# Optimization experiments

Hardware: AMD Instinct MI355X
Metric: run time of the kernel (lower is better)

The kernel has to match this reference:

```python
import jax, jax.numpy as jnp
import numpy as np
from jax import lax

DN = ('NCHW', 'OIHW', 'NCHW')

def _conv(x, w, b):
    y = lax.conv_general_dilated(x, w, (1, 1), 'SAME', dimension_numbers=DN)
    return y + b[None, :, None, None]

def setup_inputs() -> dict:
    key = jax.random.key(0)
    ks = jax.random.split(key, 12)
    B, C, H, W = 8, 32, 128, 128
    Cb, INT, K, FK = 64, 64, 3, 3
    inp = {
        'z': jax.random.normal(ks[0], (B, C, H, W), jnp.float32),
        'backbone': jax.random.normal(ks[1], (B, Cb, H, W), jnp.float32),
        'mem_stab': jax.random.normal(ks[2], (B, C, H, W), jnp.float32),
        'mem_unstab': jax.random.normal(ks[3], (B, C, H, W), jnp.float32),
        'w0': jax.random.normal(ks[4], (INT, Cb + 3 * C, K, K), jnp.float32) * 0.05,
        'b0': jnp.zeros((INT,), jnp.float32),
        'w1': jax.random.normal(ks[5], (INT, INT, K, K), jnp.float32) * 0.05,
        'b1': jnp.zeros((INT,), jnp.float32),
        'w2': jax.random.normal(ks[6], (INT, INT, K, K), jnp.float32) * 0.05,
        'b2': jnp.zeros((INT,), jnp.float32),
        'w_last': jax.random.normal(ks[7], (C * FK * FK, INT, K, K), jnp.float32) * 0.05,
        'b_last': jnp.full((C * FK * FK,), -4.0, jnp.float32),
        'fusion_kernel_size': FK,
    }
    return inp

def reference(z, backbone, mem_stab, mem_unstab, w0, b0, w1, b1, w2, b2, w_last, b_last, fusion_kernel_size):
    B, C, H, W = z.shape
    k = int(fusion_kernel_size)
    p = k * k
    # controller conv stack (LeakyReLU slope 0.01, matching nn.LeakyReLU default)
    q = jnp.concatenate([backbone, z, mem_stab, mem_unstab], axis=1)
    q = jax.nn.leaky_relu(_conv(q, w0, b0), 0.01)
    q = jax.nn.leaky_relu(_conv(q, w1, b1), 0.01)
    q = jax.nn.leaky_relu(_conv(q, w2, b2), 0.01)
    # fusion head -> [B, C, p, HW]
    head = _conv(q, w_last, b_last).reshape(B, C, p, H * W)
    # softmax over p kernel positions + one extra logit-0 slot for z itself
    eta = jax.nn.softmax(jnp.concatenate([head, jnp.zeros_like(head[:, :, :1])], axis=2), axis=2)
    # unfold(mem_stab, k, padding=k//2): patches ordered (c, kh, kw) like torch unfold
    pad = k // 2
    mpad = jnp.pad(mem_stab, ((0, 0), (0, 0), (pad, pad), (pad, pad)))
    patches = jnp.stack([mpad[:, :, i:i + H, j:j + W] for i in range(k) for j in range(k)], axis=2)
    patches = patches.reshape(B, C, p, H * W)
    z_flat = z.reshape(B, C, H * W)
    z_stab = (patches * eta[:, :, :p]).sum(axis=2) + eta[:, :, p] * z_flat
    return z_stab.reshape(B, C, H, W)
```

## Files before the change

### kernel.cpp

```cpp
#include <hip/hip_runtime.h>
#include <hip/hip_fp16.h>

typedef _Float16 half8 __attribute__((ext_vector_type(8)));
typedef _Float16 half4v __attribute__((ext_vector_type(4)));
typedef float floatx4 __attribute__((ext_vector_type(4)));

#define HW 128
#define IMG (HW * HW)
#define PH 130
#define WP 200

typedef __attribute__((address_space(3))) _Float16 lds_f16;
typedef __attribute__((address_space(1))) const _Float16 glb_f16;
__device__ __forceinline__ void gload16(const _Float16* g, _Float16* l) {
    __builtin_amdgcn_global_load_lds((glb_f16*)g, (lds_f16*)l, 16, 0, 0);
}

__global__ void pack_w_all(const float* __restrict__ w0, const float* __restrict__ w1,
                           const float* __restrict__ w2, const float* __restrict__ wl,
                           _Float16* __restrict__ p0, _Float16* __restrict__ p1,
                           _Float16* __restrict__ p2, _Float16* __restrict__ pl) {
    int idx = blockIdx.x * 256 + threadIdx.x;
    if (idx < 92160) {
        int local = idx;
        int o = local / 1440;
        int rem = local % 1440;
        int c = rem / 9;
        int t = rem % 9;
        int oh = o >> 5, n = (o >> 4) & 1, l15 = o & 15;
        int cb = c >> 5, l4 = (c >> 3) & 3, e = c & 7;
        int frag = (t * 5 + cb) * 2 + n;
        p0[(size_t)oh * 46080 + frag * 512 + (l4 * 16 + l15) * 8 + e] =
            (_Float16)w0[local];
        return;
    }
    const float* w; _Float16* p; int C; int local;
    if (idx < 129024)      { w = w1; p = p1; C = 64;  local = idx - 92160; }
    else if (idx < 165888) { w = w2; p = p2; C = 64;  local = idx - 129024; }
    else if (idx < 331776) { w = wl; p = pl; C = 64;  local = idx - 165888; }
    else return;
    int o = local / (C * 9);
    int rem = local % (C * 9);
    int c = rem / 9;
    int t = rem % 9;
    p[(o * 9 + t) * C + c] = (_Float16)w[local];
}

__device__ __forceinline__ void zero_halo(_Float16* P, int C, int id) {
    int nvec = C / 8;
    int b = id / (516 * nvec);
    int r = id % (516 * nvec);
    int cell = r / nvec;
    int v = r % nvec;
    int hh, ww;
    if (cell < 130)      { hh = 0;   ww = cell; }
    else if (cell < 260) { hh = 129; ww = cell - 130; }
    else if (cell < 388) { hh = cell - 260 + 1; ww = 0; }
    else                 { hh = cell - 388 + 1; ww = 129; }
    half8 z8 = {};
    *reinterpret_cast<half8*>(P + (((size_t)b * PH + hh) * PH + ww) * C + v * 8) = z8;
}

__global__ void zero_pads_pre(_Float16* __restrict__ X0, _Float16* __restrict__ Q1) {
    int id = blockIdx.x * 256 + threadIdx.x;
    if (id < 82560) zero_halo(X0, 160, id);
    else if (id < 115584) zero_halo(Q1, 64, id - 82560);
}

__global__ void zero_pads64(_Float16* __restrict__ P) {
    int id = blockIdx.x * 256 + threadIdx.x;
    if (id < 33024) zero_halo(P, 64, id);
}

__global__ __launch_bounds__(256)
void pack_in(const float* __restrict__ z, const float* __restrict__ bb,
             const float* __restrict__ ms, const float* __restrict__ mu,
             _Float16* __restrict__ X0) {
    __shared__ _Float16 lds[160 * 132];
    int b = blockIdx.x >> 7;
    int h = blockIdx.x & 127;
    int tid = threadIdx.x;

    for (int i = 0; i < 20; i++) {
        int id = i * 256 + tid;
        int c = id >> 5;
        int col = (id & 31) * 4;
        const float* src; int cs; int csz;
        if (c < 64)       { src = bb; cs = c;       csz = 64; }
        else if (c < 96)  { src = z;  cs = c - 64;  csz = 32; }
        else if (c < 128) { src = ms; cs = c - 96;  csz = 32; }
        else              { src = mu; cs = c - 128; csz = 32; }
        float4 v = *reinterpret_cast<const float4*>(
            src + ((size_t)b * csz + cs) * IMG + h * HW + col);
        half4v hv = { (_Float16)v.x, (_Float16)v.y, (_Float16)v.z, (_Float16)v.w };
        *reinterpret_cast<half4v*>(&lds[c * 132 + col]) = hv;
    }
    __syncthreads();
    _Float16* dst = X0 + (((size_t)b * PH + (h + 1)) * PH + 1) * 160;
    for (int i = 0; i < 10; i++) {
        int id = i * 256 + tid;
        int pix = id / 20;
        int c0 = (id % 20) * 8;
        half8 hv;
        #pragma unroll
        for (int e = 0; e < 8; e++) hv[e] = lds[(c0 + e) * 132 + pix];
        *reinterpret_cast<half8*>(dst + (size_t)pix * 160 + c0) = hv;
    }
}

__global__ __launch_bounds__(256, 2)
void conv3_c160(const _Float16* __restrict__ X, const _Float16* __restrict__ Wp,
                const float* __restrict__ bias, _Float16* __restrict__ Y) {
    __shared__ _Float16 xs[130 * 168];
    int b = blockIdx.x >> 7;
    int h = blockIdx.x & 127;
    int tid = threadIdx.x;
    int lane = tid & 63;
    int wave = tid >> 6;
    int ph = wave & 1;
    int oh = wave >> 1;
    int l15 = lane & 15;
    int l4  = lane >> 4;

    floatx4 acc[4][2] = {};
    half8 SA[10], SB[10];

    const _Float16* wl = Wp + (size_t)oh * 46080 + lane * 8;

#define LOADW(S, k) { \
    _Pragma("unroll") \
    for (int cb = 0; cb < 5; cb++) \
      _Pragma("unroll") \
      for (int n = 0; n < 2; n++) \
        S[cb * 2 + n] = *reinterpret_cast<const half8*>( \
            wl + (size_t)(((k) * 5 + cb) * 2 + n) * 512); }

#define STAGE160(r) { \
    const _Float16* grow = X + ((size_t)b * PH + (h + (r))) * PH * 160; \
    _Pragma("unroll") \
    for (int i = 0; i < 11; i++) { \
      int id = i * 256 + tid; \
      if (id < 2600) { \
        half8 v = *reinterpret_cast<const half8*>(grow + (size_t)id * 8); \
        *reinterpret_cast<half8*>(&xs[(id / 20) * 168 + (id % 20) * 8]) = v; \
      } } }

#define COMP160(dw, S) { \
    _Pragma("unroll") \
    for (int cb = 0; cb < 5; cb++) { \
      int kofs = cb * 32 + l4 * 8; \
      half8 af[4]; \
      _Pragma("unroll") \
      for (int m = 0; m < 4; m++) { \
        int p = ph * 64 + m * 16 + l15; \
        af[m] = *reinterpret_cast<const half8*>(&xs[(p + (dw)) * 168 + kofs]); \
      } \
      _Pragma("unroll") \
      for (int m = 0; m < 4; m++) \
        _Pragma("unroll") \
        for (int n = 0; n < 2; n++) \
          acc[m][n] = __builtin_amdgcn_mfma_f32_16x16x32_f16( \
              af[m], S[cb * 2 + n], acc[m][n], 0, 0, 0); } }

    LOADW(SA, 0);
    STAGE160(0);
    __syncthreads();
    LOADW(SB, 1);  COMP160(0, SA);
    LOADW(SA, 2);  COMP160(1, SB);
    LOADW(SB, 3);  COMP160(2, SA);
    __syncthreads();
    STAGE160(1);
    __syncthreads();
    LOADW(SA, 4);  COMP160(0, SB);
    LOADW(SB, 5);  COMP160(1, SA);
    LOADW(SA, 6);  COMP160(2, SB);
    __syncthreads();
    STAGE160(2);
    __syncthreads();
    LOADW(SB, 7);  COMP160(0, SA);
    LOADW(SA, 8);  COMP160(1, SB);
    COMP160(2, SA);

#undef LOADW
#undef STAGE160
#undef COMP160

    _Float16* dst = Y + (((size_t)b * PH + (h + 1)) * PH + 1) * 64;
    #pragma unroll
    for (int m = 0; m < 4; m++)
        #pragma unroll
        for (int n = 0; n < 2; n++) {
            int o = oh * 32 + n * 16 + l15;
            float bv = bias[o];
            #pragma unroll
            for (int q = 0; q < 4; q++) {
                int pix = ph * 64 + m * 16 + l4 * 4 + q;
                float v = acc[m][n][q] + bv;
                v = v > 0.f ? v : 0.01f * v;
                dst[(size_t)pix * 64 + o] = (_Float16)v;
            }
        }
}

__global__ __launch_bounds__(256, 3)
void conv3_c64(const _Float16* __restrict__ X, const _Float16* __restrict__ Wp,
               const float* __restrict__ bias, _Float16* __restrict__ Y) {
    __shared__ _Float16 smem[9360 + 64 * WP];
    _Float16* xs = smem;
    _Float16* wbuf = smem + 9360;
    int b = blockIdx.x >> 7;
    int h = blockIdx.x & 127;
    int tid = threadIdx.x;
    int lane = tid & 63;
    int wave = tid >> 6;
    int ph = wave & 1;
    int oh = wave >> 1;
    int l15 = lane & 15;
    int l4  = lane >> 4;

    floatx4 acc[4][2] = {};
    const _Float16* xbase = X + ((size_t)b * PH + h) * (PH * 64);

    for (int r = 0; r < 3; r++) {
        if (r) __syncthreads();
        for (int i = 0; i < 5; i++) {
            int id = i * 256 + tid;
            if (id < 1040) {
                half8 v = *reinterpret_cast<const half8*>(
                    xbase + (size_t)r * (PH * 64) + (size_t)id * 8);
                *reinterpret_cast<half8*>(&xs[(id >> 3) * 72 + (id & 7) * 8]) = v;
            }
        }
        for (int i = 0; i < 6; i++) {
            int id = i * 256 + tid;
            int o = id / 24, j = id % 24;
            half8 v = *reinterpret_cast<const half8*>(
                Wp + ((size_t)o * 9 + r * 3) * 64 + j * 8);
            *reinterpret_cast<half8*>(&wbuf[o * WP + j * 8]) = v;
        }
        __syncthreads();
        #pragma unroll
        for (int dw = 0; dw < 3; dw++)
            #pragma unroll
            for (int cb = 0; cb < 2; cb++) {
                int kofs = cb * 32 + l4 * 8;
                half8 bf[2];
                #pragma unroll
                for (int n = 0; n < 2; n++) {
                    int o = oh * 32 + n * 16 + l15;
                    bf[n] = *reinterpret_cast<const half8*>(
                        &wbuf[o * WP + dw * 64 + kofs]);
                }
                half8 af[4];
                #pragma unroll
                for (int m = 0; m < 4; m++) {
                    int p = ph * 64 + m * 16 + l15;
                    af[m] = *reinterpret_cast<const half8*>(&xs[(p + dw) * 72 + kofs]);
                }
                #pragma unroll
                for (int m = 0; m < 4; m++)
                    #pragma unroll
                    for (int n = 0; n < 2; n++)
                        acc[m][n] = __builtin_amdgcn_mfma_f32_16x16x32_f16(
                            af[m], bf[n], acc[m][n], 0, 0, 0);
            }
    }
    _Float16* dst = Y + (((size_t)b * PH + (h + 1)) * PH + 1) * 64;
    #pragma unroll
    for (int m = 0; m < 4; m++)
        #pragma unroll
        for (int n = 0; n < 2; n++) {
            int o = oh * 32 + n * 16 + l15;
            float bv = bias[o];
            #pragma unroll
            for (int q = 0; q < 4; q++) {
                int pix = ph * 64 + m * 16 + l4 * 4 + q;
                float v = acc[m][n][q] + bv;
                v = v > 0.f ? v : 0.01f * v;
                dst[(size_t)pix * 64 + o] = (_Float16)v;
            }
        }
}

__global__ __launch_bounds__(256, 3)
void head_gemm(const _Float16* __restrict__ X, const _Float16* __restrict__ Wp,
               const float* __restrict__ b_last, _Float16* __restrict__ Lg,
               int bbase) {
    __shared__ _Float16 smem[26752];
    _Float16* xs = smem;
    _Float16* wbuf = smem + 8320;
    _Float16* tb = smem;
    int blk = blockIdx.x;
    int ct = blk >> 9;
    int bi = (blk >> 7) & 3;
    int h  = blk & 127;
    int b = bbase + bi;
    int tid = threadIdx.x;
    int lane = tid & 63;
    int wave = tid >> 6;
    int pxh = wave & 1;
    int og  = wave >> 1;
    int l15 = lane & 15;
    int l4  = lane >> 4;

    floatx4 acc[4][3] = {};
    const _Float16* xbase = X + ((size_t)b * PH + h) * (PH * 64);
    const _Float16* wbase = Wp + (size_t)ct * 96 * 9 * 64;

    for (int r = 0; r < 3; r++) {
        if (r) __syncthreads();
        const _Float16* xrow = xbase + (size_t)r * (PH * 64);
        for (int i = 0; i < 5; i++) {
            int sbase = i * 256 + wave * 64;
            int s = sbase + lane;
            if (s < 1040) {
                int px = s >> 3;
                int j = (s & 7) ^ (px & 7);
                gload16(xrow + (size_t)(px * 8 + j) * 8, xs + (size_t)sbase * 8);
            }
        }
        const _Float16* wrow = wbase + r * 192;
        for (int i = 0; i < 9; i++) {
            int tbs = i * 256 + wave * 64;
            int t = tbs + lane;
            int o = t / 24, ks = t % 24;
            int k = (ks & 0x18) | ((ks & 7) ^ (o & 7));
            gload16(wrow + (size_t)(o * 576 + k * 8), wbuf + (size_t)tbs * 8);
        }
        __syncthreads();
        #pragma unroll
        for (int dw = 0; dw < 3; dw++)
            #pragma unroll
            for (int cb = 0; cb < 2; cb++) {
                int kb = dw * 8 + cb * 4 + l4;
                half8 bf[3];
                #pragma unroll
                for (int n = 0; n < 3; n++) {
                    int ol = og * 48 + n * 16 + l15;
                    int ksw = (kb & 0x18) | ((kb & 7) ^ (ol & 7));
                    bf[n] = *reinterpret_cast<const half8*>(&wbuf[ol * 192 + ksw * 8]);
                }
                int j = cb * 4 + l4;
                half8 af[4];
                #pragma unroll
                for (int m = 0; m < 4; m++) {
                    int px = pxh * 64 + m * 16 + l15 + dw;
                    af[m] = *reinterpret_cast<const half8*>(
                        &xs[px * 64 + (j ^ (px & 7)) * 8]);
                }
                #pragma unroll
                for (int m = 0; m < 4; m++)
                    #pragma unroll
                    for (int n = 0; n < 3; n++)
                        acc[m][n] = __builtin_amdgcn_mfma_f32_16x16x32_f16(
                            af[m], bf[n], acc[m][n], 0, 0, 0);
            }
    }
    __syncthreads();

    #pragma unroll
    for (int m = 0; m < 4; m++)
        #pragma unroll
        for (int n = 0; n < 3; n++) {
            int od = og * 48 + n * 16 + l15;
            float bv = b_last[ct * 96 + od];
            half4v hv;
            #pragma unroll
            for (int q = 0; q < 4; q++) hv[q] = (_Float16)(acc[m][n][q] + bv);
            *reinterpret_cast<half4v*>(&tb[od * 132 + pxh * 64 + m * 16 + l4 * 4]) = hv;
        }
    __syncthreads();

    _Float16* dst = Lg + (((size_t)bi * 128 + h) * 288 + (size_t)ct * 96) * 128;
    #pragma unroll
    for (int i = 0; i < 6; i++) {
        int id = i * 256 + tid;
        int od = id >> 4;
        int sl = id & 15;
        half8 v = *reinterpret_cast<const half8*>(&tb[od * 132 + sl * 8]);
        *reinterpret_cast<half8*>(dst + (size_t)od * 128 + sl * 8) = v;
    }
}

__global__ __launch_bounds__(256)
void fuse_sm(const _Float16* __restrict__ Lg, const float* __restrict__ ms,
             const float* __restrict__ zin, float* __restrict__ out, int bbase) {
    int blk = blockIdx.x;
    int bi = blk >> 11;
    int c  = (blk >> 6) & 31;
    int hp = blk & 63;
    int tid = threadIdx.x;
    int h = hp * 2 + (tid >> 7);
    int w = tid & 127;
    int b = bbase + bi;

    const _Float16* lrow = Lg + (((size_t)bi * 128 + h) * 288 + (size_t)c * 9) * 128 + w;
    float L[9];
    float mx = 0.f;
    #pragma unroll
    for (int j = 0; j < 9; j++) { L[j] = (float)lrow[j * 128]; mx = fmaxf(mx, L[j]); }
    float ez = __expf(-mx);
    float sum = ez;
    float e[9];
    #pragma unroll
    for (int j = 0; j < 9; j++) { e[j] = __expf(L[j] - mx); sum += e[j]; }
    float inv = 1.f / sum;
    const float* msb = ms + ((size_t)b * 32 + c) * IMG;
    float accv = ez * inv * zin[((size_t)b * 32 + c) * IMG + h * HW + w];
    #pragma unroll
    for (int kh = 0; kh < 3; kh++) {
        int h2 = h + kh - 1;
        int h2c = min(max(h2, 0), 127);
        bool okh = (unsigned)h2 < 128u;
        #pragma unroll
        for (int kw = 0; kw < 3; kw++) {
            int w2 = w + kw - 1;
            int w2c = min(max(w2, 0), 127);
            bool okw = (unsigned)w2 < 128u;
            float mv = msb[h2c * HW + w2c];
            accv += e[kh * 3 + kw] * inv * ((okh && okw) ? mv : 0.f);
        }
    }
    out[((size_t)b * 32 + c) * IMG + h * HW + w] = accv;
}

extern "C" void kernel_launch(void* const* d_in, const int* in_sizes, int n_in,
                              void* d_out, int out_size, void* d_ws, size_t ws_size,
                              hipStream_t stream) {
    const float* z  = (const float*)d_in[0];
    const float* bb = (const float*)d_in[1];
    const float* ms = (const float*)d_in[2];
    const float* mu = (const float*)d_in[3];
    const float* w0 = (const float*)d_in[4];
    const float* b0 = (const float*)d_in[5];
    const float* w1 = (const float*)d_in[6];
    const float* b1 = (const float*)d_in[7];
    const float* w2 = (const float*)d_in[8];
    const float* b2 = (const float*)d_in[9];
    const float* wl = (const float*)d_in[10];
    const float* bl = (const float*)d_in[11];

    char* ws = (char*)d_ws;
    _Float16* Wp0 = (_Float16*)(ws + 0);
    _Float16* Wp1 = (_Float16*)(ws + 184320);
    _Float16* Wp2 = (_Float16*)(ws + 258048);
    _Float16* WpL = (_Float16*)(ws + 331776);
    _Float16* BufA = (_Float16*)(ws + 663552);
    _Float16* BufB = (_Float16*)(ws + 43927552);

    _Float16* X0 = BufA;
    _Float16* Q1 = BufB;
    _Float16* Q2 = BufA;
    _Float16* Q3 = BufB;
    _Float16* Lg = BufA;

    pack_w_all<<<(331776 + 255) / 256, 256, 0, stream>>>(w0, w1, w2, wl, Wp0, Wp1, Wp2, WpL);
    zero_pads_pre<<<(115584 + 255) / 256, 256, 0, stream>>>(X0, Q1);
    pack_in<<<1024, 256, 0, stream>>>(z, bb, ms, mu, X0);

    conv3_c160<<<1024, 256, 0, stream>>>(X0, Wp0, b0, Q1);
    zero_pads64<<<(33024 + 255) / 256, 256, 0, stream>>>(Q2);
    conv3_c64<<<1024, 256, 0, stream>>>(Q1, Wp1, b1, Q2);
    conv3_c64<<<1024, 256, 0, stream>>>(Q2, Wp2, b2, Q3);

    head_gemm<<<1536, 256, 0, stream>>>(Q3, WpL, bl, Lg, 0);
    fuse_sm<<<8192, 256, 0, stream>>>(Lg, ms, z, (float*)d_out, 0);
    head_gemm<<<1536, 256, 0, stream>>>(Q3, WpL, bl, Lg, 4);
    fuse_sm<<<8192, 256, 0, stream>>>(Lg, ms, z, (float*)d_out, 4);
}
```

Measured before the change: 189.1 us.

## Prefetch next input row into registers during compute and raise occupancy

The first conv kernel now loads the next input row from global memory into registers while the current row's MFMAs run, then writes it to LDS after a barrier, instead of staging synchronously. The weight double buffer is collapsed to a single buffer so the prefetch registers fit, and launch bounds are raised to 3 blocks per CU. The LDS row pitch shrinks from 168 to 164 halves, which changes bank mapping and reduces LDS use. The risks are register spills under the tighter occupancy bound, and weight loads becoming exposed now that the double buffer is gone.

```diff
diff --git a/kernel.cpp b/kernel.cpp
--- a/kernel.cpp
+++ b/kernel.cpp
@@ -9,6 +9,7 @@
 #define IMG (HW * HW)
 #define PH 130
 #define WP 200
+#define XP 164
 
 typedef __attribute__((address_space(3))) _Float16 lds_f16;
 typedef __attribute__((address_space(1))) const _Float16 glb_f16;
@@ -108,10 +109,10 @@
     }
 }
 
-__global__ __launch_bounds__(256, 2)
+__global__ __launch_bounds__(256, 3)
 void conv3_c160(const _Float16* __restrict__ X, const _Float16* __restrict__ Wp,
                 const float* __restrict__ bias, _Float16* __restrict__ Y) {
-    __shared__ _Float16 xs[130 * 168];
+    __shared__ _Float16 xs[130 * XP];
     int b = blockIdx.x >> 7;
     int h = blockIdx.x & 127;
     int tid = threadIdx.x;
@@ -123,29 +124,37 @@
     int l4  = lane >> 4;
 
     floatx4 acc[4][2] = {};
-    half8 SA[10], SB[10];
+    half8 SA[10];
+    half8 R[11];
 
     const _Float16* wl = Wp + (size_t)oh * 46080 + lane * 8;
 
-#define LOADW(S, k) { \
+#define LOADW(k) { \
     _Pragma("unroll") \
     for (int cb = 0; cb < 5; cb++) \
       _Pragma("unroll") \
       for (int n = 0; n < 2; n++) \
-        S[cb * 2 + n] = *reinterpret_cast<const half8*>( \
+        SA[cb * 2 + n] = *reinterpret_cast<const half8*>( \
             wl + (size_t)(((k) * 5 + cb) * 2 + n) * 512); }
 
-#define STAGE160(r) { \
+#define STAGE_LOAD(r) { \
     const _Float16* grow = X + ((size_t)b * PH + (h + (r))) * PH * 160; \
     _Pragma("unroll") \
     for (int i = 0; i < 11; i++) { \
       int id = i * 256 + tid; \
-      if (id < 2600) { \
-        half8 v = *reinterpret_cast<const half8*>(grow + (size_t)id * 8); \
-        *reinterpret_cast<half8*>(&xs[(id / 20) * 168 + (id % 20) * 8]) = v; \
-      } } }
-
-#define COMP160(dw, S) { \
+      if (id < 2600) \
+        R[i] = *reinterpret_cast<const half8*>(grow + (size_t)id * 8); \
+    } }
+
+#define STAGE_WRITE() { \
+    _Pragma("unroll") \
+    for (int i = 0; i < 11; i++) { \
+      int id = i * 256 + tid; \
+      if (id < 2600) \
+        *reinterpret_cast<half8*>(&xs[(id / 20) * XP + (id % 20) * 8]) = R[i]; \
+    } }
+
+#define COMP160(dw) { \
     _Pragma("unroll") \
     for (int cb = 0; cb < 5; cb++) { \
       int kofs = cb * 32 + l4 * 8; \
@@ -153,36 +162,40 @@
       _Pragma("unroll") \
       for (int m = 0; m < 4; m++) { \
         int p = ph * 64 + m * 16 + l15; \
-        af[m] = *reinterpret_cast<const half8*>(&xs[(p + (dw)) * 168 + kofs]); \
+        af[m] = *reinterpret_cast<const half8*>(&xs[(p + (dw)) * XP + kofs]); \
       } \
       _Pragma("unroll") \
       for (int m = 0; m < 4; m++) \
         _Pragma("unroll") \
         for (int n = 0; n < 2; n++) \
           acc[m][n] = __builtin_amdgcn_mfma_f32_16x16x32_f16( \
-              af[m], S[cb * 2 + n], acc[m][n], 0, 0, 0); } }
-
-    LOADW(SA, 0);
-    STAGE160(0);
-    __syncthreads();
-    LOADW(SB, 1);  COMP160(0, SA);
-    LOADW(SA, 2);  COMP160(1, SB);
-    LOADW(SB, 3);  COMP160(2, SA);
-    __syncthreads();
-    STAGE160(1);
-    __syncthreads();
-    LOADW(SA, 4);  COMP160(0, SB);
-    LOADW(SB, 5);  COMP160(1, SA);
-    LOADW(SA, 6);  COMP160(2, SB);
-    __syncthreads();
-    STAGE160(2);
-    __syncthreads();
-    LOADW(SB, 7);  COMP160(0, SA);
-    LOADW(SA, 8);  COMP160(1, SB);
-    COMP160(2, SA);
+              af[m], SA[cb * 2 + n], acc[m][n], 0, 0, 0); } }
+
+    STAGE_LOAD(0);
+    LOADW(0);
+    STAGE_WRITE();
+    __syncthreads();
+    STAGE_LOAD(1);
+    COMP160(0);  LOADW(1);
+    COMP160(1);  LOADW(2);
+    COMP160(2);  LOADW(3);
+    __syncthreads();
+    STAGE_WRITE();
+    __syncthreads();
+    STAGE_LOAD(2);
+    COMP160(0);  LOADW(4);
+    COMP160(1);  LOADW(5);
+    COMP160(2);  LOADW(6);
+    __syncthreads();
+    STAGE_WRITE();
+    __syncthreads();
+    COMP160(0);  LOADW(7);
+    COMP160(1);  LOADW(8);
+    COMP160(2);
 
 #undef LOADW
-#undef STAGE160
+#undef STAGE_LOAD
+#undef STAGE_WRITE
 #undef COMP160
 
     _Float16* dst = Y + (((size_t)b * PH + (h + 1)) * PH + 1) * 64;
```

Result: no change. 191.8 us (+1.4%).
